# Kernel optimization log

Measured on AMD Instinct MI355X. Metric: run time of the kernel, lower is better.

The kernel has to match this reference:

```python
import jax, jax.numpy as jnp
import numpy as np

NEG = -1e9
ALPHA = 0.2  # LeakyReLU slope


def layer_norm(x, scale, bias, eps=1e-5):
    mu = jnp.mean(x, axis=-1, keepdims=True)
    var = jnp.mean(jnp.square(x - mu), axis=-1, keepdims=True)
    return (x - mu) * jax.lax.rsqrt(var + eps) * scale + bias


def gat_layer(x, adj, W, a):
    # x: (b, n, f_in); W: (h, f_in, d_k); a: (h, 2*d_k, 1); adj: (b, n, n) int
    d_k = W.shape[-1]
    h = jnp.einsum('bni,hio->bhno', x, W)            # (b, h, n, d_k)
    a_src = a[:, :d_k, 0]                            # (h, d_k)
    a_dst = a[:, d_k:, 0]                            # (h, d_k)
    # e[b,h,i,j] = leakyrelu(a_src.h_i + a_dst.h_j) -- split form of a.[h_i||h_j]
    src = jnp.einsum('bhnd,hd->bhn', h, a_src)
    dst = jnp.einsum('bhnd,hd->bhn', h, a_dst)
    e = jax.nn.leaky_relu(src[:, :, :, None] + dst[:, :, None, :], ALPHA)
    e = jnp.where(adj[:, None, :, :] == 0, NEG, e)   # mask non-edges
    att = jax.nn.softmax(e, axis=-1)                 # (b, h, n, n)
    return jnp.einsum('bhnm,bhmd->bhnd', att, h)     # (b, h, n, d_k)


def setup_inputs() -> dict:
    key = jax.random.key(0)
    ks = jax.random.split(key, 8)
    B, N, F_IN, HID, OUT, H = 4, 2048, 128, 256, 256, 4
    dk1 = HID // H
    dk2 = OUT // H
    xavier = lambda k, shp: jax.random.uniform(
        k, shp, jnp.float32, -1.0, 1.0) * np.sqrt(6.0 / (shp[-2] + shp[-1]))
    return {
        'node_features': jax.random.normal(ks[0], (B, N, F_IN), jnp.float32),
        'adjacency_matrix': jax.random.randint(ks[1], (B, N, N), 0, 2, jnp.int32),
        'Wp': jax.random.normal(ks[2], (F_IN, HID), jnp.float32) / np.sqrt(F_IN),
        'bp': jnp.zeros((HID,), jnp.float32),
        'W1': xavier(ks[3], (H, HID, dk1)),
        'a1': xavier(ks[4], (H, 2 * dk1, 1)),
        'ln1_s': jnp.ones((HID,), jnp.float32),
        'ln1_b': jnp.zeros((HID,), jnp.float32),
        'W2': xavier(ks[5], (H, HID, dk2)),
        'a2': xavier(ks[6], (H, 2 * dk2, 1)),
        'ln2_s': jnp.ones((dk2,), jnp.float32),
        'ln2_b': jnp.zeros((dk2,), jnp.float32),
    }


def reference(node_features, adjacency_matrix, Wp, bp, W1, a1, ln1_s, ln1_b,
              W2, a2, ln2_s, ln2_b):
    # input projection (dropout is identity in eval mode)
    x = node_features @ Wp + bp                       # (b, n, hid)
    b, n, _ = x.shape

    # layer 1: concat heads, LN, ELU, residual
    hp = gat_layer(x, adjacency_matrix, W1, a1)       # (b, h, n, dk1)
    x1 = hp.reshape(b, n, -1)                         # memory-order reshape (matches torch .view)
    x1 = layer_norm(x1, ln1_s, ln1_b)
    x1 = jax.nn.elu(x1)
    x = x + x1                                        # same shape -> residual

    # layer 2: mean over heads, LN
    hp = gat_layer(x, adjacency_matrix, W2, a2)       # (b, h, n, dk2)
    x2 = hp.mean(axis=1)                              # (b, n, dk2)
    x2 = layer_norm(x2, ln2_s, ln2_b)
    return x2
```

## Files before the change

kernel.cpp:

```cpp
#include <hip/hip_runtime.h>
#include <hip/hip_bf16.h>
#include <hip/hip_fp16.h>

#define BB   4
#define NN   2048
#define FIN  128
#define HD   256
#define NH   4
#define DK   64
#define NEGV (-1000000000.0f)
#define LOG2E 1.4426950408889634f

typedef _Float16 f16x8 __attribute__((ext_vector_type(8)));
typedef float    f32x16 __attribute__((ext_vector_type(16)));
typedef unsigned long long u64;

__device__ __forceinline__ int SWZ9(int b){ return b ^ (((b >> 9) & 7) << 4); }

__device__ __forceinline__ float fexp2(float x){
#if __has_builtin(__builtin_amdgcn_exp2f)
  return __builtin_amdgcn_exp2f(x);
#else
  return __exp2f(x);
#endif
}

__device__ __forceinline__ f16x8 pack8(float4 a, float4 b){
  f16x8 r;
  r[0]=(_Float16)a.x; r[1]=(_Float16)a.y; r[2]=(_Float16)a.z; r[3]=(_Float16)a.w;
  r[4]=(_Float16)b.x; r[5]=(_Float16)b.y; r[6]=(_Float16)b.z; r[7]=(_Float16)b.w;
  return r;
}

__global__ void __launch_bounds__(256) k_setup(const float* __restrict__ nf,
                                               const float* __restrict__ Wp,
                                               const float* __restrict__ bp,
                                               const int* __restrict__ adj,
                                               const float* __restrict__ W1,
                                               const float* __restrict__ a1,
                                               const float* __restrict__ W2,
                                               const float* __restrict__ a2,
                                               float* __restrict__ x,
                                               u64* __restrict__ maskT,
                                               _Float16* __restrict__ WT,
                                               float* __restrict__ aS){
  __shared__ __align__(16) float xs[16][FIN];
  int bid = blockIdx.x;
  if (bid < 512){
    int r0 = bid * 16;
    int c = threadIdx.x;
    for (int k = threadIdx.x; k < 16*FIN/4; k += 256){
      int r = k >> 5; int cc = (k & 31) * 4;
      *(float4*)&xs[r][cc] = *(const float4*)&nf[(size_t)(r0 + r)*FIN + cc];
    }
    __syncthreads();
    float acc[16];
    float bv = bp[c];
    #pragma unroll
    for (int r = 0; r < 16; ++r) acc[r] = bv;
    #pragma unroll 4
    for (int i = 0; i < FIN; i += 4){
      float w0 = Wp[(i+0)*HD + c];
      float w1 = Wp[(i+1)*HD + c];
      float w2 = Wp[(i+2)*HD + c];
      float w3 = Wp[(i+3)*HD + c];
      #pragma unroll
      for (int r = 0; r < 16; ++r){
        float4 xv = *(const float4*)&xs[r][i];
        acc[r] = fmaf(xv.x, w0, acc[r]);
        acc[r] = fmaf(xv.y, w1, acc[r]);
        acc[r] = fmaf(xv.z, w2, acc[r]);
        acc[r] = fmaf(xv.w, w3, acc[r]);
      }
    }
    #pragma unroll
    for (int r = 0; r < 16; ++r) x[(size_t)(r0 + r)*HD + c] = acc[r];
  } else if (bid < 2560){
    int w = threadIdx.x >> 6, lane = threadIdx.x & 63;
    int row = (bid - 512)*4 + w;
    int b = row >> 11, n = row & (NN-1);
    const int* ar = adj + (size_t)row*NN;
    #pragma unroll 4
    for (int mt = 0; mt < 32; ++mt){
      u64 bal = __ballot(ar[mt*64 + lane] != 0);
      if (lane == 0) maskT[(size_t)(b*32 + mt)*NN + n] = bal;
    }
  } else {
    int q = bid - 2560;
    int lay = q >> 2, hh = q & 3;
    const float* W = (lay ? W2 : W1) + (size_t)hh*HD*DK;
    const float* a = (lay ? a2 : a1) + (size_t)hh*2*DK;
    _Float16* wt = WT + ((size_t)lay*4 + hh)*64*256;
    float* as = aS + ((size_t)lay*4 + hh)*128;
    int t = threadIdx.x;
    int d = t & 63;
    #pragma unroll 4
    for (int it = 0; it < 64; ++it){
      int k = it*4 + (t >> 6);
      wt[(size_t)d*256 + k] = (_Float16)W[(size_t)k*DK + d];
    }
    if (t < 128) as[t] = a[t] * LOG2E;
  }
}

__global__ void __launch_bounds__(256) k_head3(const float* __restrict__ x,
                                               const _Float16* __restrict__ WT,
                                               const float* __restrict__ aS,
                                               _Float16* __restrict__ hT,
                                               float* __restrict__ src,
                                               float* __restrict__ dst){
  int nt = blockIdx.x & 31;
  int bh = blockIdx.x >> 5;
  int b = bh >> 2, hh = bh & 3;
  int n0 = nt * 64;
  int t = threadIdx.x;
  int w = t >> 6, l = t & 63, lh = l >> 5, l5 = l & 31;
  int wr = w >> 1, wc = w & 1;

  __shared__ __align__(16) char sm[66560];

  {
    int r = t >> 2, ks = (t & 3) * 64;
    const float* xp = &x[((size_t)(b*NN) + n0 + r)*HD + ks];
    #pragma unroll
    for (int u = 0; u < 8; ++u){
      float4 v0 = *(const float4*)&xp[u*8];
      float4 v1 = *(const float4*)&xp[u*8 + 4];
      *(f16x8*)&sm[SWZ9(r*512 + (ks + u*8)*2)] = pack8(v0, v1);
    }
  }
  {
    int d = t >> 2, ks = (t & 3) * 64;
    const _Float16* wp = WT + ((size_t)hh*64 + d)*256 + ks;
    #pragma unroll
    for (int u = 0; u < 8; ++u){
      f16x8 v = *(const f16x8*)&wp[u*8];
      *(f16x8*)&sm[SWZ9(32768 + d*512 + (ks + u*8)*2)] = v;
    }
  }
  __syncthreads();

  f32x16 accA = {}, accB = {};
  #pragma unroll
  for (int kk = 0; kk < 16; kk += 2){
    int kb0 = (kk*16 + lh*8)*2;
    int kb1 = ((kk+1)*16 + lh*8)*2;
    f16x8 A0 = *(const f16x8*)&sm[SWZ9((wr*32 + l5)*512 + kb0)];
    f16x8 B0 = *(const f16x8*)&sm[SWZ9(32768 + (wc*32 + l5)*512 + kb0)];
    f16x8 A1 = *(const f16x8*)&sm[SWZ9((wr*32 + l5)*512 + kb1)];
    f16x8 B1 = *(const f16x8*)&sm[SWZ9(32768 + (wc*32 + l5)*512 + kb1)];
    accA = __builtin_amdgcn_mfma_f32_32x32x16_f16(A0, B0, accA, 0, 0, 0);
    accB = __builtin_amdgcn_mfma_f32_32x32x16_f16(A1, B1, accB, 0, 0, 0);
  }
  f32x16 acc = accA + accB;

  __syncthreads();
  _Float16* ls = (_Float16*)sm;
  int col = wc*32 + l5;
  float as = aS[((size_t)hh)*128 + col];
  float ad = aS[((size_t)hh)*128 + 64 + col];
  float* sd = (float*)(sm + 65536);
  #pragma unroll
  for (int g = 0; g < 16; ++g){
    int row = wr*32 + (g & 3) + 8*(g >> 2) + 4*lh;
    ls[col*80 + row] = (_Float16)acc[g];
    float sv = acc[g] * as;
    float dv = acc[g] * ad;
    #pragma unroll
    for (int o = 16; o >= 1; o >>= 1){ sv += __shfl_xor(sv, o); dv += __shfl_xor(dv, o); }
    if (l5 == 0){
      sd[wc*64 + row]        = sv;
      sd[128 + wc*64 + row]  = dv;
    }
  }
  __syncthreads();
  int dd = t >> 2, part = t & 3;
  f16x8 o0 = *(const f16x8*)&ls[dd*80 + part*16];
  f16x8 o1 = *(const f16x8*)&ls[dd*80 + part*16 + 8];
  int base = part*1024 + (dd >> 5)*512 + (dd & 31)*16;
  _Float16* op = hT + (size_t)bh*131072 + (size_t)nt*4096 + base;
  *(f16x8*)op = o0;
  *(f16x8*)(op + 8) = o1;
  if (t < 64){
    src[bh*NN + n0 + t] = sd[t] + sd[64 + t];
    dst[bh*NN + n0 + t] = sd[128 + t] + sd[192 + t];
  }
}

__global__ void __launch_bounds__(256, 6) k_attn8(const float* __restrict__ src,
                                                  const float* __restrict__ dst,
                                                  const _Float16* __restrict__ hT,
                                                  const u64* __restrict__ maskT,
                                                  _Float16* __restrict__ accB,
                                                  float* __restrict__ psB){
  int ms = blockIdx.x & 1;
  int rb = (blockIdx.x >> 1) & 63;
  int bh = blockIdx.x >> 7;
  int b  = bh >> 2;
  int n0 = rb * 32;
  int t = threadIdx.x;
  int w = t >> 6, l = t & 63;
  int lh = l >> 5, l5 = l & 31;

  __shared__ __align__(16) char smem[9728];
  __shared__ float rs[4][32];
  __shared__ float red[4];
  float* dstS = (float*)smem;
  float* cs   = (float*)smem;

  {
    const float* dp = dst + bh*NN;
    float4 a = *(const float4*)&dp[t*4];
    float4 bq = *(const float4*)&dp[1024 + t*4];
    float mloc = fmaxf(fmaxf(fmaxf(a.x,a.y), fmaxf(a.z,a.w)),
                       fmaxf(fmaxf(bq.x,bq.y), fmaxf(bq.z,bq.w)));
    *(float4*)&dstS[t*4] = ms ? bq : a;
    #pragma unroll
    for (int o = 32; o >= 1; o >>= 1) mloc = fmaxf(mloc, __shfl_xor(mloc, o));
    if (l == 0) red[w] = mloc;
  }
  __syncthreads();
  float Mbh = fmaxf(fmaxf(red[0], red[1]), fmaxf(red[2], red[3]));
  float srcv = src[bh*NN + n0 + l5];
  float bv = srcv + Mbh;
  float bnd = fmaxf(bv, 0.2f*bv);
  float psum = 0.f;
  f32x16 acc0 = {}, acc1 = {};

  int kb = w*16 + lh*8;
  const u64* mp = maskT + (size_t)(b*32 + ms*16)*NN + n0 + l5;
  const char* gB = (const char*)hT + (size_t)bh*262144 + ms*131072
                   + w*2048 + l5*32 + lh*16;
  u64 mk = *mp;
  f16x8 B0 = *(const f16x8*)gB;
  f16x8 B1 = *(const f16x8*)(gB + 1024);
  float4 dq0 = *(const float4*)&dstS[kb];
  float4 dq1 = *(const float4*)&dstS[kb + 4];

  for (int mt = 0; mt < 16; ++mt){
    u64 mkN = mk; f16x8 B0N = B0, B1N = B1; float4 dq0N = dq0, dq1N = dq1;
    if (mt < 15){
      mp += NN; gB += 8192;
      mkN = *mp;
      B0N = *(const f16x8*)gB;
      B1N = *(const f16x8*)(gB + 1024);
      dq0N = *(const float4*)&dstS[(mt+1)*64 + kb];
      dq1N = *(const float4*)&dstS[(mt+1)*64 + kb + 4];
    }
    unsigned bits = (unsigned)(mk >> kb) & 0xFFu;
    float dvals[8] = {dq0.x,dq0.y,dq0.z,dq0.w,dq1.x,dq1.y,dq1.z,dq1.w};
    f16x8 A;
    #pragma unroll
    for (int i = 0; i < 8; ++i){
      float e = srcv + dvals[i];
      e = fmaxf(e, 0.2f*e);
      e = ((bits >> i) & 1u) ? e : NEGV;
      float p = fexp2(e - bnd);
      psum += p;
      A[i] = (_Float16)p;
    }
    acc0 = __builtin_amdgcn_mfma_f32_32x32x16_f16(A, B0, acc0, 0, 0, 0);
    acc1 = __builtin_amdgcn_mfma_f32_32x32x16_f16(A, B1, acc1, 0, 0, 0);
    mk = mkN; B0 = B0N; B1 = B1N; dq0 = dq0N; dq1 = dq1N;
  }

  psum += __shfl_xor(psum, 32);
  if (l < 32) rs[w][l5] = psum;
  __syncthreads();
  _Float16* accO = accB + (size_t)ms*2097152;
  float* psO  = psB + (size_t)ms*32768;
  if (t < 32) psO[bh*NN + n0 + t] = rs[0][t] + rs[1][t] + rs[2][t] + rs[3][t];
  #pragma unroll 1
  for (int ww = 1; ww < 4; ++ww){
    if (w == ww){
      float* base = cs + l*36;
      *(f32x16*)(base)      = acc0;
      *(f32x16*)(base + 16) = acc1;
    }
    __syncthreads();
    if (w == 0){
      const float* base = cs + l*36;
      acc0 += *(const f32x16*)(base);
      acc1 += *(const f32x16*)(base + 16);
    }
    __syncthreads();
  }
  if (w == 0){
    #pragma unroll
    for (int g = 0; g < 16; ++g){
      int row = (g & 3) + 8*(g >> 2) + 4*lh;
      size_t o = ((size_t)bh*NN + n0 + row)*DK;
      accO[o + l5]      = (_Float16)acc0[g];
      accO[o + 32 + l5] = (_Float16)acc1[g];
    }
  }
}

__global__ void __launch_bounds__(256) k_ln1(const _Float16* __restrict__ a0,
                                             const _Float16* __restrict__ a1,
                                             const float* __restrict__ p0,
                                             const float* __restrict__ p1,
                                             const float* __restrict__ sc,
                                             const float* __restrict__ bi,
                                             float* __restrict__ x){
  int j = blockIdx.x & (NN-1);
  int b = blockIdx.x / NN;
  int c = threadIdx.x;
  int w = c >> 6, l = c & 63;
  int hh = j >> 9;
  int node = ((j & 511) << 2) + w;
  size_t ridx = (size_t)(b*NH + hh)*NN + node;
  float inv = 1.f / (p0[ridx] + p1[ridx]);
  size_t idx = ridx*DK + l;
  float v = ((float)a0[idx] + (float)a1[idx]) * inv;
  __shared__ float red[8];
  float s = v;
  #pragma unroll
  for (int o = 32; o >= 1; o >>= 1) s += __shfl_xor(s, o);
  if (l == 0) red[w] = s;
  __syncthreads();
  float mu = (red[0]+red[1]+red[2]+red[3]) * (1.f/HD);
  float dv = v - mu;
  float q = dv*dv;
  #pragma unroll
  for (int o = 32; o >= 1; o >>= 1) q += __shfl_xor(q, o);
  if (l == 0) red[4+w] = q;
  __syncthreads();
  float var = (red[4]+red[5]+red[6]+red[7]) * (1.f/HD);
  float ln = dv * rsqrtf(var + 1e-5f) * sc[c] + bi[c];
  float el = (ln > 0.f) ? ln : (__expf(ln) - 1.f);
  x[(size_t)blockIdx.x*HD + c] += el;
}

__global__ void __launch_bounds__(256) k_final(const _Float16* __restrict__ a0,
                                               const _Float16* __restrict__ a1,
                                               const float* __restrict__ p0,
                                               const float* __restrict__ p1,
                                               const float* __restrict__ sc,
                                               const float* __restrict__ bi,
                                               float* __restrict__ out){
  int w = threadIdx.x >> 6; int d = threadIdx.x & 63;
  int bn = blockIdx.x*4 + w;
  int b = bn / NN; int n = bn & (NN-1);
  float v = 0.f;
  #pragma unroll
  for (int hh = 0; hh < NH; ++hh){
    size_t ridx = (size_t)(b*NH + hh)*NN + n;
    float inv = 1.f / (p0[ridx] + p1[ridx]);
    size_t idx = ridx*DK + d;
    v += ((float)a0[idx] + (float)a1[idx]) * inv;
  }
  v *= 0.25f;
  float s = v;
  #pragma unroll
  for (int o = 32; o >= 1; o >>= 1) s += __shfl_xor(s, o);
  float mu = s * (1.f/DK);
  float dv = v - mu;
  float q = dv*dv;
  #pragma unroll
  for (int o = 32; o >= 1; o >>= 1) q += __shfl_xor(q, o);
  float var = q * (1.f/DK);
  float ln = dv * rsqrtf(var + 1e-5f) * sc[d] + bi[d];
  out[(size_t)bn*DK + d] = ln;
}

extern "C" void kernel_launch(void* const* d_in, const int* in_sizes, int n_in,
                              void* d_out, int out_size, void* d_ws, size_t ws_size,
                              hipStream_t stream){
  const float* nf   = (const float*)d_in[0];
  const int*   adj  = (const int*)d_in[1];
  const float* Wp   = (const float*)d_in[2];
  const float* bp   = (const float*)d_in[3];
  const float* W1   = (const float*)d_in[4];
  const float* a1   = (const float*)d_in[5];
  const float* ln1s = (const float*)d_in[6];
  const float* ln1b = (const float*)d_in[7];
  const float* W2   = (const float*)d_in[8];
  const float* a2   = (const float*)d_in[9];
  const float* ln2s = (const float*)d_in[10];
  const float* ln2b = (const float*)d_in[11];

  float* ws   = (float*)d_ws;
  float* x    = ws;
  _Float16* accF = (_Float16*)(ws + 2097152);
  float* srcb = ws + 3*2097152;
  float* dstb = srcb + 32768;
  float* psA  = dstb + 32768;
  _Float16* hT = (_Float16*)(psA + 2*32768);
  u64* maskT  = (u64*)(hT + 2097152);
  _Float16* WT = (_Float16*)(maskT + 262144);
  float* aS   = (float*)(WT + 131072);

  _Float16* accH0 = accF;
  _Float16* accH1 = accF + 2097152;
  float* psH0  = psA;
  float* psH1  = psA + 32768;

  k_setup<<<2568,         256, 0, stream>>>(nf, Wp, bp, adj, W1, a1, W2, a2,
                                            x, maskT, WT, aS);
  k_head3<<<BB*NH*NN/64,  256, 0, stream>>>(x, WT,         aS,       hT, srcb, dstb);
  k_attn8<<<BB*NH*NN/16,  256, 0, stream>>>(srcb, dstb, hT, maskT, accF, psA);
  k_ln1  <<<BB*NN,        256, 0, stream>>>(accH0, accH1, psH0, psH1, ln1s, ln1b, x);
  k_head3<<<BB*NH*NN/64,  256, 0, stream>>>(x, WT + 65536, aS + 512, hT, srcb, dstb);
  k_attn8<<<BB*NH*NN/16,  256, 0, stream>>>(srcb, dstb, hT, maskT, accF, psA);
  k_final<<<BB*NN/4,      256, 0, stream>>>(accH0, accH1, psH0, psH1, ln2s, ln2b, (float*)d_out);
}
```

Measured before the change: 137.6 us.

## Fuse input projection into head kernel via MFMA, prepack weights in fragment layout

Removes the scalar FP32 input-projection path from the setup kernel. The layer-1 head kernel now computes x = nf@Wp+bp with f16 MFMA, staged in shared memory, and the hh==0 block writes x for the residual. Each of the 4 head blocks per tile recomputes the projection. Weights W1/W2/Wp are prepacked into MFMA B-fragment order so they are read straight from global memory instead of staged in LDS, which shrinks shared memory. The adjacency-to-bitmask conversion now uses int4 loads with nibble packing and shuffle-OR reduction instead of per-element ballots. Trade-offs: the projection is computed redundantly per head and now runs in fp16, which loses precision compared with the FP32 version.

```diff
diff --git a/kernel.cpp b/kernel.cpp
--- a/kernel.cpp
+++ b/kernel.cpp
@@ -16,6 +16,7 @@
 typedef unsigned long long u64;
 
 __device__ __forceinline__ int SWZ9(int b){ return b ^ (((b >> 9) & 7) << 4); }
+__device__ __forceinline__ int SWZ8(int b){ return b ^ (((b >> 8) & 7) << 4); }
 
 __device__ __forceinline__ float fexp2(float x){
 #if __has_builtin(__builtin_amdgcn_exp2f)
@@ -32,80 +33,71 @@
   return r;
 }
 
-__global__ void __launch_bounds__(256) k_setup(const float* __restrict__ nf,
+__global__ void __launch_bounds__(256) k_setup(const int* __restrict__ adj,
                                                const float* __restrict__ Wp,
-                                               const float* __restrict__ bp,
-                                               const int* __restrict__ adj,
                                                const float* __restrict__ W1,
                                                const float* __restrict__ a1,
                                                const float* __restrict__ W2,
                                                const float* __restrict__ a2,
-                                               float* __restrict__ x,
                                                u64* __restrict__ maskT,
-                                               _Float16* __restrict__ WT,
+                                               _Float16* __restrict__ WTF,
+                                               _Float16* __restrict__ WpF,
                                                float* __restrict__ aS){
-  __shared__ __align__(16) float xs[16][FIN];
   int bid = blockIdx.x;
-  if (bid < 512){
-    int r0 = bid * 16;
-    int c = threadIdx.x;
-    for (int k = threadIdx.x; k < 16*FIN/4; k += 256){
-      int r = k >> 5; int cc = (k & 31) * 4;
-      *(float4*)&xs[r][cc] = *(const float4*)&nf[(size_t)(r0 + r)*FIN + cc];
-    }
-    __syncthreads();
-    float acc[16];
-    float bv = bp[c];
-    #pragma unroll
-    for (int r = 0; r < 16; ++r) acc[r] = bv;
-    #pragma unroll 4
-    for (int i = 0; i < FIN; i += 4){
-      float w0 = Wp[(i+0)*HD + c];
-      float w1 = Wp[(i+1)*HD + c];
-      float w2 = Wp[(i+2)*HD + c];
-      float w3 = Wp[(i+3)*HD + c];
+  int t = threadIdx.x;
+  if (bid < 2048){
+    int w = t >> 6, lane = t & 63;
+    int row = bid*4 + w;
+    int b = row >> 11, n = row & (NN-1);
+    const int4* ar = (const int4*)(adj + (size_t)row*NN);
+    int g = lane >> 4, q = lane & 15;
+    #pragma unroll 2
+    for (int step = 0; step < 8; ++step){
+      int4 v = ar[step*64 + lane];
+      unsigned nib = (unsigned)((v.x!=0) | ((v.y!=0)<<1) | ((v.z!=0)<<2) | ((v.w!=0)<<3));
+      unsigned lo = (q < 8) ? (nib << (q*4)) : 0u;
+      unsigned hi = (q < 8) ? 0u : (nib << ((q-8)*4));
       #pragma unroll
-      for (int r = 0; r < 16; ++r){
-        float4 xv = *(const float4*)&xs[r][i];
-        acc[r] = fmaf(xv.x, w0, acc[r]);
-        acc[r] = fmaf(xv.y, w1, acc[r]);
-        acc[r] = fmaf(xv.z, w2, acc[r]);
-        acc[r] = fmaf(xv.w, w3, acc[r]);
+      for (int off = 1; off < 16; off <<= 1){
+        lo |= __shfl_xor(lo, off);
+        hi |= __shfl_xor(hi, off);
       }
-    }
-    #pragma unroll
-    for (int r = 0; r < 16; ++r) x[(size_t)(r0 + r)*HD + c] = acc[r];
-  } else if (bid < 2560){
-    int w = threadIdx.x >> 6, lane = threadIdx.x & 63;
-    int row = (bid - 512)*4 + w;
-    int b = row >> 11, n = row & (NN-1);
-    const int* ar = adj + (size_t)row*NN;
-    #pragma unroll 4
-    for (int mt = 0; mt < 32; ++mt){
-      u64 bal = __ballot(ar[mt*64 + lane] != 0);
-      if (lane == 0) maskT[(size_t)(b*32 + mt)*NN + n] = bal;
-    }
-  } else {
-    int q = bid - 2560;
-    int lay = q >> 2, hh = q & 3;
+      if (q == 0) maskT[(size_t)(b*32 + step*4 + g)*NN + n] = ((u64)hi << 32) | lo;
+    }
+  } else if (bid < 2056){
+    int qq = bid - 2048;
+    int lay = qq >> 2, hh = qq & 3;
     const float* W = (lay ? W2 : W1) + (size_t)hh*HD*DK;
     const float* a = (lay ? a2 : a1) + (size_t)hh*2*DK;
-    _Float16* wt = WT + ((size_t)lay*4 + hh)*64*256;
-    float* as = aS + ((size_t)lay*4 + hh)*128;
-    int t = threadIdx.x;
-    int d = t & 63;
+    _Float16* wf = WTF + (size_t)qq*32*512;
+    int j = t*2;
+    int l5 = j >> 4, lh = (j >> 3) & 1, e = j & 7;
     #pragma unroll 4
-    for (int it = 0; it < 64; ++it){
-      int k = it*4 + (t >> 6);
-      wt[(size_t)d*256 + k] = (_Float16)W[(size_t)k*DK + d];
-    }
-    if (t < 128) as[t] = a[t] * LOG2E;
-  }
-}
-
-__global__ void __launch_bounds__(256) k_head3(const float* __restrict__ x,
-                                               const _Float16* __restrict__ WT,
+    for (int f = 0; f < 32; ++f){
+      int kk = f >> 1, dh = f & 1;
+      wf[f*512 + j]     = (_Float16)W[(kk*16 + lh*8 + e    )*DK + dh*32 + l5];
+      wf[f*512 + j + 1] = (_Float16)W[(kk*16 + lh*8 + e + 1)*DK + dh*32 + l5];
+    }
+    if (t < 128) aS[(size_t)qq*128 + t] = a[t] * LOG2E;
+  } else {
+    int kk = bid - 2056;
+    int j = t*2;
+    int l5 = j >> 4, lh = (j >> 3) & 1, e = j & 7;
+    #pragma unroll 4
+    for (int cs = 0; cs < 8; ++cs){
+      WpF[(kk*8 + cs)*512 + j]     = (_Float16)Wp[(kk*16 + lh*8 + e    )*HD + cs*32 + l5];
+      WpF[(kk*8 + cs)*512 + j + 1] = (_Float16)Wp[(kk*16 + lh*8 + e + 1)*HD + cs*32 + l5];
+    }
+  }
+}
+
+template<int L1>
+__global__ void __launch_bounds__(256) k_head4(const float* __restrict__ xin,
+                                               const _Float16* __restrict__ WpF,
+                                               const _Float16* __restrict__ WTF,
                                                const float* __restrict__ aS,
+                                               const float* __restrict__ bp,
+                                               float* __restrict__ xout,
                                                _Float16* __restrict__ hT,
                                                float* __restrict__ src,
                                                float* __restrict__ dst){
@@ -117,49 +109,87 @@
   int w = t >> 6, l = t & 63, lh = l >> 5, l5 = l & 31;
   int wr = w >> 1, wc = w & 1;
 
-  __shared__ __align__(16) char sm[66560];
-
-  {
+  __shared__ __align__(16) char sm[50176];
+
+  if (L1){
+    {
+      int r = t >> 2, c0 = (t & 3) * 32;
+      const float* np = xin + ((size_t)(b*NN) + n0 + r)*FIN + c0;
+      #pragma unroll
+      for (int u = 0; u < 4; ++u){
+        float4 v0 = *(const float4*)&np[u*8];
+        float4 v1 = *(const float4*)&np[u*8 + 4];
+        *(f16x8*)&sm[32768 + SWZ8(r*256 + (c0 + u*8)*2)] = pack8(v0, v1);
+      }
+    }
+    __syncthreads();
+    f32x16 p00 = {}, p01 = {}, p10 = {}, p11 = {};
+    #pragma unroll
+    for (int kk = 0; kk < 8; ++kk){
+      int ab = (kk*16 + lh*8)*2;
+      f16x8 A0 = *(const f16x8*)&sm[32768 + SWZ8(l5*256 + ab)];
+      f16x8 A1 = *(const f16x8*)&sm[32768 + SWZ8((32 + l5)*256 + ab)];
+      const char* bf = (const char*)WpF + (size_t)(kk*8 + w*2)*1024 + l5*32 + lh*16;
+      f16x8 B0 = *(const f16x8*)bf;
+      f16x8 B1 = *(const f16x8*)(bf + 1024);
+      p00 = __builtin_amdgcn_mfma_f32_32x32x16_f16(A0, B0, p00, 0, 0, 0);
+      p01 = __builtin_amdgcn_mfma_f32_32x32x16_f16(A0, B1, p01, 0, 0, 0);
+      p10 = __builtin_amdgcn_mfma_f32_32x32x16_f16(A1, B0, p10, 0, 0, 0);
+      p11 = __builtin_amdgcn_mfma_f32_32x32x16_f16(A1, B1, p11, 0, 0, 0);
+    }
+    int c0a = w*64 + l5;
+    float bp0 = bp[c0a], bp1 = bp[c0a + 32];
+    size_t ro = ((size_t)(b*NN) + n0)*HD;
+    #pragma unroll
+    for (int g = 0; g < 16; ++g){
+      int rr = (g & 3) + 8*(g >> 2) + 4*lh;
+      float v00 = p00[g] + bp0, v01 = p01[g] + bp1;
+      float v10 = p10[g] + bp0, v11 = p11[g] + bp1;
+      *(_Float16*)&sm[SWZ9(rr*512 + c0a*2)]             = (_Float16)v00;
+      *(_Float16*)&sm[SWZ9(rr*512 + (c0a + 32)*2)]      = (_Float16)v01;
+      *(_Float16*)&sm[SWZ9((rr+32)*512 + c0a*2)]        = (_Float16)v10;
+      *(_Float16*)&sm[SWZ9((rr+32)*512 + (c0a + 32)*2)] = (_Float16)v11;
+      if (hh == 0){
+        xout[ro + (size_t)rr*HD + c0a]           = v00;
+        xout[ro + (size_t)rr*HD + c0a + 32]      = v01;
+        xout[ro + (size_t)(rr+32)*HD + c0a]      = v10;
+        xout[ro + (size_t)(rr+32)*HD + c0a + 32] = v11;
+      }
+    }
+    __syncthreads();
+  } else {
     int r = t >> 2, ks = (t & 3) * 64;
-    const float* xp = &x[((size_t)(b*NN) + n0 + r)*HD + ks];
+    const float* xp = &xin[((size_t)(b*NN) + n0 + r)*HD + ks];
     #pragma unroll
     for (int u = 0; u < 8; ++u){
       float4 v0 = *(const float4*)&xp[u*8];
       float4 v1 = *(const float4*)&xp[u*8 + 4];
       *(f16x8*)&sm[SWZ9(r*512 + (ks + u*8)*2)] = pack8(v0, v1);
     }
-  }
-  {
-    int d = t >> 2, ks = (t & 3) * 64;
-    const _Float16* wp = WT + ((size_t)hh*64 + d)*256 + ks;
-    #pragma unroll
-    for (int u = 0; u < 8; ++u){
-      f16x8 v = *(const f16x8*)&wp[u*8];
-      *(f16x8*)&sm[SWZ9(32768 + d*512 + (ks + u*8)*2)] = v;
-    }
-  }
-  __syncthreads();
-
-  f32x16 accA = {}, accB = {};
+    __syncthreads();
+  }
+
+  f32x16 hA = {}, hB = {};
+  const char* wtb = (const char*)WTF + (size_t)hh*32768 + wc*1024 + l5*32 + lh*16;
   #pragma unroll
   for (int kk = 0; kk < 16; kk += 2){
-    int kb0 = (kk*16 + lh*8)*2;
-    int kb1 = ((kk+1)*16 + lh*8)*2;
-    f16x8 A0 = *(const f16x8*)&sm[SWZ9((wr*32 + l5)*512 + kb0)];
-    f16x8 B0 = *(const f16x8*)&sm[SWZ9(32768 + (wc*32 + l5)*512 + kb0)];
-    f16x8 A1 = *(const f16x8*)&sm[SWZ9((wr*32 + l5)*512 + kb1)];
-    f16x8 B1 = *(const f16x8*)&sm[SWZ9(32768 + (wc*32 + l5)*512 + kb1)];
-    accA = __builtin_amdgcn_mfma_f32_32x32x16_f16(A0, B0, accA, 0, 0, 0);
-    accB = __builtin_amdgcn_mfma_f32_32x32x16_f16(A1, B1, accB, 0, 0, 0);
-  }
-  f32x16 acc = accA + accB;
+    int ab0 = (kk*16 + lh*8)*2;
+    int ab1 = ((kk+1)*16 + lh*8)*2;
+    f16x8 A0 = *(const f16x8*)&sm[SWZ9((wr*32 + l5)*512 + ab0)];
+    f16x8 A1 = *(const f16x8*)&sm[SWZ9((wr*32 + l5)*512 + ab1)];
+    f16x8 B0 = *(const f16x8*)(wtb + (size_t)kk*2048);
+    f16x8 B1 = *(const f16x8*)(wtb + (size_t)(kk+1)*2048);
+    hA = __builtin_amdgcn_mfma_f32_32x32x16_f16(A0, B0, hA, 0, 0, 0);
+    hB = __builtin_amdgcn_mfma_f32_32x32x16_f16(A1, B1, hB, 0, 0, 0);
+  }
+  f32x16 acc = hA + hB;
 
   __syncthreads();
   _Float16* ls = (_Float16*)sm;
   int col = wc*32 + l5;
-  float as = aS[((size_t)hh)*128 + col];
-  float ad = aS[((size_t)hh)*128 + 64 + col];
-  float* sd = (float*)(sm + 65536);
+  float as = aS[(size_t)hh*128 + col];
+  float ad = aS[(size_t)hh*128 + 64 + col];
+  float* sd = (float*)(sm + 49152);
   #pragma unroll
   for (int g = 0; g < 16; ++g){
     int row = wr*32 + (g & 3) + 8*(g >> 2) + 4*lh;
@@ -169,8 +199,8 @@
     #pragma unroll
     for (int o = 16; o >= 1; o >>= 1){ sv += __shfl_xor(sv, o); dv += __shfl_xor(dv, o); }
     if (l5 == 0){
-      sd[wc*64 + row]        = sv;
-      sd[128 + wc*64 + row]  = dv;
+      sd[wc*64 + row]       = sv;
+      sd[128 + wc*64 + row] = dv;
     }
   }
   __syncthreads();
@@ -388,20 +418,21 @@
   float* psA  = dstb + 32768;
   _Float16* hT = (_Float16*)(psA + 2*32768);
   u64* maskT  = (u64*)(hT + 2097152);
-  _Float16* WT = (_Float16*)(maskT + 262144);
-  float* aS   = (float*)(WT + 131072);
+  _Float16* WTF = (_Float16*)(maskT + 262144);
+  _Float16* WpF = WTF + 131072;
+  float* aS   = (float*)(WpF + 32768);
 
   _Float16* accH0 = accF;
   _Float16* accH1 = accF + 2097152;
   float* psH0  = psA;
   float* psH1  = psA + 32768;
 
-  k_setup<<<2568,         256, 0, stream>>>(nf, Wp, bp, adj, W1, a1, W2, a2,
-                                            x, maskT, WT, aS);
-  k_head3<<<BB*NH*NN/64,  256, 0, stream>>>(x, WT,         aS,       hT, srcb, dstb);
-  k_attn8<<<BB*NH*NN/16,  256, 0, stream>>>(srcb, dstb, hT, maskT, accF, psA);
-  k_ln1  <<<BB*NN,        256, 0, stream>>>(accH0, accH1, psH0, psH1, ln1s, ln1b, x);
-  k_head3<<<BB*NH*NN/64,  256, 0, stream>>>(x, WT + 65536, aS + 512, hT, srcb, dstb);
-  k_attn8<<<BB*NH*NN/16,  256, 0, stream>>>(srcb, dstb, hT, maskT, accF, psA);
-  k_final<<<BB*NN/4,      256, 0, stream>>>(accH0, accH1, psH0, psH1, ln2s, ln2b, (float*)d_out);
-}
+  k_setup   <<<2064,        256, 0, stream>>>(adj, Wp, W1, a1, W2, a2,
+                                              maskT, WTF, WpF, aS);
+  k_head4<1><<<BB*NH*NN/64, 256, 0, stream>>>(nf, WpF, WTF,        aS,       bp, x, hT, srcb, dstb);
+  k_attn8   <<<BB*NH*NN/16, 256, 0, stream>>>(srcb, dstb, hT, maskT, accF, psA);
+  k_ln1     <<<BB*NN,       256, 0, stream>>>(accH0, accH1, psH0, psH1, ln1s, ln1b, x);
+  k_head4<0><<<BB*NH*NN/64, 256, 0, stream>>>(x, WpF, WTF + 65536, aS + 512, bp, x, hT, srcb, dstb);
+  k_attn8   <<<BB*NH*NN/16, 256, 0, stream>>>(srcb, dstb, hT, maskT, accF, psA);
+  k_final   <<<BB*NN/4,     256, 0, stream>>>(accH0, accH1, psH0, psH1, ln2s, ln2b, (float*)d_out);
+}
```

New measurement: 120.1 us. -12.7%, faster.
